# Kernel tuning notes

Hardware: AMD Instinct MI355X
Metric: run time of the kernel (lower is better)

Reference implementation:

```python
import jax, jax.numpy as jnp
import numpy as np

B, N, E, H, DEPTH = 2, 2048, 1024, 8, 12
D = E // H // 2  # head_dim = 64
LN_EPS = 1e-5


def setup_inputs() -> dict:
    key = jax.random.key(0)
    ks = jax.random.split(key, 10)
    w = lambda k: jax.random.normal(k, (E, E), jnp.float32) * (E ** -0.5)
    lp = lambda k: jax.random.normal(k, (D,), jnp.float32) * 0.1
    return {
        "x": jax.random.normal(ks[0], (B, N, E), jnp.float32),
        "Wq": w(ks[1]), "Wk": w(ks[2]), "Wv": w(ks[3]), "Wo": w(ks[4]),
        "lq1": lp(ks[5]), "lk1": lp(ks[6]), "lq2": lp(ks[7]), "lk2": lp(ks[8]),
        "ln_g": jnp.ones((2 * D,), jnp.float32),
        "ln_b": jnp.zeros((2 * D,), jnp.float32),
    }


def reference(x, Wq, Wk, Wv, Wo, lq1, lk1, lq2, lk2, ln_g, ln_b):
    b, n, e = x.shape
    lam_init = 0.8 - 0.6 * np.exp(-0.3 * DEPTH)  # lambda_init_fn(depth)
    # projections; split into 2H half-heads of dim D for q,k; H heads of dim 2D for v
    q = (x @ Wq).reshape(b, n, 2 * H, D).transpose(0, 2, 1, 3) * (D ** -0.5)  # [b,2H,n,D]
    k = (x @ Wk).reshape(b, n, 2 * H, D).transpose(0, 2, 1, 3)                # [b,2H,n,D]
    v = (x @ Wv).reshape(b, n, H, 2 * D).transpose(0, 2, 1, 3)                # [b,H,n,2D]
    scores = jnp.einsum('bhqd,bhkd->bhqk', q, k)                              # [b,2H,n,n]
    attn = jax.nn.softmax(scores, axis=-1).reshape(b, H, 2, n, n)
    lam = jnp.exp(jnp.sum(lq1 * lk1)) - jnp.exp(jnp.sum(lq2 * lk2)) + lam_init
    w_diff = attn[:, :, 0] - lam * attn[:, :, 1]                              # [b,H,n,n]
    o = jnp.einsum('bhqk,bhkd->bhqd', w_diff, v)                              # [b,H,n,2D]
    # per-head LayerNorm over channel dim 2D
    mu = o.mean(-1, keepdims=True)
    var = ((o - mu) ** 2).mean(-1, keepdims=True)
    o = (o - mu) * jax.lax.rsqrt(var + LN_EPS) * ln_g + ln_b
    o = o.transpose(0, 2, 1, 3).reshape(b, n, e)
    return o @ Wo
```

## Files before the change

### kernel.cpp

```cpp
#include <hip/hip_runtime.h>
#include <hip/hip_bf16.h>
#include <math.h>

#define B_ 2
#define N_ 2048
#define E_ 1024
#define H_ 8

typedef __attribute__((ext_vector_type(8))) short frag8;
typedef __attribute__((ext_vector_type(4))) float f32x4;
typedef __attribute__((ext_vector_type(16))) float f32x16;
typedef __attribute__((ext_vector_type(8))) unsigned short u16x8;

constexpr float LAM_INIT = 0.7836057665316245f;
constexpr float LOG2E = 1.4426950408889634f;
constexpr float EXP2_GUARD = -23.083120654f;

static __device__ __forceinline__ float fast_exp2(float x) {
#if __has_builtin(__builtin_amdgcn_exp2f)
  return __builtin_amdgcn_exp2f(x);
#else
  return exp2f(x);
#endif
}

static __device__ __forceinline__ ushort f2bf(float f) {
  union { float f; unsigned u; } v; v.f = f;
  unsigned r = (v.u + 0x7FFFu + ((v.u >> 16) & 1u)) >> 16;
  return (ushort)r;
}

static __device__ __forceinline__ unsigned pkbf(float a, float b) {
  __hip_bfloat162 h = __float22bfloat162_rn(make_float2(a, b));
  return *(unsigned*)&h;
}

static __device__ __forceinline__ void async16(const void* g, void* l) {
  __builtin_amdgcn_global_load_lds((const __attribute__((address_space(1))) void*)g,
                                   (__attribute__((address_space(3))) void*)l, 16, 0, 0);
}

static __device__ __forceinline__ frag8 mkfrag(unsigned p0, unsigned p1,
                                               unsigned p2, unsigned p3) {
  auto r02 = __builtin_amdgcn_permlane32_swap((int)p0, (int)p2, false, false);
  auto r13 = __builtin_amdgcn_permlane32_swap((int)p1, (int)p3, false, false);
  union { unsigned u[4]; frag8 f; } u;
  u.u[0] = (unsigned)r02[0];
  u.u[1] = (unsigned)r13[0];
  u.u[2] = (unsigned)r02[1];
  u.u[3] = (unsigned)r13[1];
  return u.f;
}

__global__ __launch_bounds__(256) void prep_kernel(
    const float* __restrict__ x,
    const float* __restrict__ Wq, const float* __restrict__ Wk,
    const float* __restrict__ Wv, const float* __restrict__ Wo,
    const float* __restrict__ lq1, const float* __restrict__ lk1,
    const float* __restrict__ lq2, const float* __restrict__ lk2,
    ushort* __restrict__ xb, ushort* __restrict__ wqkvt, ushort* __restrict__ wot,
    float* __restrict__ lam_out) {
  __shared__ ushort t[64][72];
  const int bx = blockIdx.x;
  const int tid = threadIdx.x;
  if (bx < 2048) {
    int i = bx * 256 + tid;
    const float4* sp = (const float4*)x + (size_t)i * 2;
    float4 a = sp[0], b = sp[1];
    u16x8 o;
    o[0] = f2bf(a.x); o[1] = f2bf(a.y); o[2] = f2bf(a.z); o[3] = f2bf(a.w);
    o[4] = f2bf(b.x); o[5] = f2bf(b.y); o[6] = f2bf(b.z); o[7] = f2bf(b.w);
    *(u16x8*)(xb + (size_t)i * 8) = o;
  } else if (bx < 3072) {
    int idx = bx - 2048;
    int sel = idx >> 8, rem = idx & 255;
    const float* W = (sel == 0) ? Wq : (sel == 1) ? Wk : (sel == 2) ? Wv : Wo;
    ushort* Wt = (sel < 3) ? (wqkvt + (size_t)sel * 1048576) : wot;
    const int c0 = (rem & 15) * 64, r0 = (rem >> 4) * 64;
    {
      int r = tid >> 2, cc = (tid & 3) * 16;
      const float* sp = W + (size_t)(r0 + r) * 1024 + c0 + cc;
      #pragma unroll
      for (int j = 0; j < 4; j++) {
        float4 a = *(const float4*)(sp + j * 4);
        t[cc + j * 4 + 0][r] = f2bf(a.x);
        t[cc + j * 4 + 1][r] = f2bf(a.y);
        t[cc + j * 4 + 2][r] = f2bf(a.z);
        t[cc + j * 4 + 3][r] = f2bf(a.w);
      }
    }
    __syncthreads();
    int c = tid >> 2, rr = (tid & 3) * 16;
    ushort* dp = Wt + (size_t)(c0 + c) * 1024 + r0 + rr;
    *(u16x8*)dp = *(u16x8*)&t[c][rr];
    *(u16x8*)(dp + 8) = *(u16x8*)&t[c][rr + 8];
  } else {
    if (tid < 64) {
      float t1 = lq1[tid] * lk1[tid];
      float t2 = lq2[tid] * lk2[tid];
      #pragma unroll
      for (int off = 32; off > 0; off >>= 1) {
        t1 += __shfl_down(t1, off);
        t2 += __shfl_down(t2, off);
      }
      if (tid == 0) lam_out[0] = expf(t1) - expf(t2) + LAM_INIT;
    }
  }
}

__global__ __launch_bounds__(256) void gemm_qkv(const ushort* __restrict__ xb,
                                                const ushort* __restrict__ wqkvt,
                                                ushort* __restrict__ qkb,
                                                ushort* __restrict__ vtb, float qscale) {
  __shared__ ushort As[4096];
  __shared__ ushort Bs[4096];
  const int id0 = blockIdx.x;
  const int id = (id0 & 7) * 96 + (id0 >> 3);
  const ushort* A; const ushort* Bt; ushort* C;
  int m0, n0, ldc;
  float sc;
  if (id < 512) {
    m0 = (id >> 4) * 128; n0 = (id & 15) * 128;
    A = xb; Bt = wqkvt; C = qkb; ldc = 2048;
    sc = (n0 < 1024) ? qscale : 1.0f;
  } else {
    int id2 = id - 512;
    m0 = (id2 & 7) * 128; n0 = (id2 >> 3) * 128;
    A = wqkvt + 2 * 1048576; Bt = xb; C = vtb; ldc = 4096;
    sc = 1.0f;
  }
  const int tid = threadIdx.x;
  const int w = tid >> 6, l = tid & 63;
  const int quad = l >> 4, col16 = l & 15;
  const int wm = (w & 1) * 64, wn = (w >> 1) * 64;
  const int lrow = l >> 2, lcol = (l & 3) * 8;

  f32x4 acc[4][4];
  #pragma unroll
  for (int mt = 0; mt < 4; mt++)
    #pragma unroll
    for (int nt = 0; nt < 4; nt++) acc[mt][nt] = (f32x4){0.f, 0.f, 0.f, 0.f};

  for (int k0 = 0; k0 < 1024; k0 += 32) {
    __syncthreads();
    #pragma unroll
    for (int i = 0; i < 4; i++) {
      int s = w * 4 + i;
      if (s < 8) {
        const ushort* gp = A + (size_t)(m0 + s * 16 + lrow) * 1024 + k0 + lcol;
        async16(gp, (char*)As + s * 1024);
      } else {
        int s2 = s - 8;
        const ushort* gp = Bt + (size_t)(n0 + s2 * 16 + lrow) * 1024 + k0 + lcol;
        async16(gp, (char*)Bs + s2 * 1024);
      }
    }
    __syncthreads();
    frag8 af[4], bfr[4];
    #pragma unroll
    for (int mt = 0; mt < 4; mt++)
      af[mt] = *(const frag8*)((const char*)As + (wm + mt * 16 + col16) * 64 + quad * 16);
    #pragma unroll
    for (int nt = 0; nt < 4; nt++)
      bfr[nt] = *(const frag8*)((const char*)Bs + (wn + nt * 16 + col16) * 64 + quad * 16);
    #pragma unroll
    for (int mt = 0; mt < 4; mt++)
      #pragma unroll
      for (int nt = 0; nt < 4; nt++)
        acc[mt][nt] = __builtin_amdgcn_mfma_f32_16x16x32_bf16(af[mt], bfr[nt], acc[mt][nt], 0, 0, 0);
  }

  #pragma unroll
  for (int mt = 0; mt < 4; mt++)
    #pragma unroll
    for (int r = 0; r < 4; r++) {
      int m = m0 + wm + mt * 16 + quad * 4 + r;
      #pragma unroll
      for (int nt = 0; nt < 4; nt++) {
        int n = n0 + wn + nt * 16 + col16;
        C[(size_t)m * ldc + n] = f2bf(acc[mt][nt][r] * sc);
      }
    }
}

__global__ __launch_bounds__(256) void gemm_out(const ushort* __restrict__ A,
                                                const ushort* __restrict__ Bt,
                                                float* __restrict__ Cp) {
  __shared__ ushort As[2048];
  __shared__ ushort Bs[4096];
  const int tid = threadIdx.x;
  const int w = tid >> 6, l = tid & 63;
  const int quad = l >> 4, col16 = l & 15;
  const int m0 = blockIdx.y * 64, n0 = blockIdx.x * 128;
  const int wm = (w & 1) * 32, wn = (w >> 1) * 64;
  const int lrow = l >> 2, lcol = (l & 3) * 8;

  f32x4 acc[2][4];
  #pragma unroll
  for (int mt = 0; mt < 2; mt++)
    #pragma unroll
    for (int nt = 0; nt < 4; nt++) acc[mt][nt] = (f32x4){0.f, 0.f, 0.f, 0.f};

  for (int k0 = 0; k0 < 1024; k0 += 32) {
    __syncthreads();
    #pragma unroll
    for (int i = 0; i < 3; i++) {
      int s = w * 3 + i;
      if (s < 4) {
        const ushort* gp = A + (size_t)(m0 + s * 16 + lrow) * 1024 + k0 + lcol;
        async16(gp, (char*)As + s * 1024);
      } else {
        int s2 = s - 4;
        const ushort* gp = Bt + (size_t)(n0 + s2 * 16 + lrow) * 1024 + k0 + lcol;
        async16(gp, (char*)Bs + s2 * 1024);
      }
    }
    __syncthreads();
    frag8 af[2], bfr[4];
    #pragma unroll
    for (int mt = 0; mt < 2; mt++)
      af[mt] = *(const frag8*)((const char*)As + (wm + mt * 16 + col16) * 64 + quad * 16);
    #pragma unroll
    for (int nt = 0; nt < 4; nt++)
      bfr[nt] = *(const frag8*)((const char*)Bs + (wn + nt * 16 + col16) * 64 + quad * 16);
    #pragma unroll
    for (int mt = 0; mt < 2; mt++)
      #pragma unroll
      for (int nt = 0; nt < 4; nt++)
        acc[mt][nt] = __builtin_amdgcn_mfma_f32_16x16x32_bf16(af[mt], bfr[nt], acc[mt][nt], 0, 0, 0);
  }

  #pragma unroll
  for (int mt = 0; mt < 2; mt++)
    #pragma unroll
    for (int r = 0; r < 4; r++) {
      int m = m0 + wm + mt * 16 + quad * 4 + r;
      #pragma unroll
      for (int nt = 0; nt < 4; nt++) {
        int n = n0 + wn + nt * 16 + col16;
        Cp[(size_t)m * 1024 + n] = acc[mt][nt][r];
      }
    }
}

__global__ __launch_bounds__(512, 2) void flash_kernel(const ushort* __restrict__ qk,
                                                       const ushort* __restrict__ vt,
                                                       const float* __restrict__ lam_p,
                                                       const float* __restrict__ ln_g,
                                                       const float* __restrict__ ln_b,
                                                       ushort* __restrict__ onorm) {
  const int L = blockIdx.x;
  const int hb = (L & 7) | (((L >> 3) & 1) << 3);
  const int qb = L >> 4;
  const int h = hb & 7, b = hb >> 3;

  const int tid = threadIdx.x;
  const int w = tid >> 6;
  const int hsel = w >> 2;
  const int h2 = 2 * h + hsel;
  const int lane31 = tid & 31, half = (tid & 63) >> 5;
  const int qloc = (w & 3) * 32 + lane31;
  const int i0 = qb * 128 + (w & 3) * 32;

  __shared__ char smem[131584];
  char* A0 = smem;
  char* A1 = smem + 32768;
  char* B0 = smem + 65536;
  char* B1 = smem + 98304;
  float* epi = (float*)smem;
  float* epi_l = (float*)(smem + 131072);

  const float lam = lam_p[0];

  frag8 qf[4];
  #pragma unroll
  for (int chk = 0; chk < 4; chk++) {
    const ushort* qp = qk + (size_t)(b * N_ + i0 + lane31) * 2048 +
                       h2 * 64 + chk * 16 + half * 8;
    qf[chk] = *(const frag8*)qp;
  }

  f32x16 o_[4];
  #pragma unroll
  for (int cm = 0; cm < 4; cm++)
    #pragma unroll
    for (int i = 0; i < 16; i++) o_[cm][i] = 0.f;
  float la0 = 0.f, la1 = 0.f;

  auto stage = [&](int k0, char* buf) {
    {
      int row = tid >> 3, sch = (tid & 7) ^ (row & 7);
      const ushort* kg = qk + (size_t)(b * N_ + k0 + row) * 2048 + 1024 + (2 * h) * 64 + sch * 8;
      async16(kg, buf + w * 1024);
    }
    {
      int row = tid >> 3, sch = (tid & 7) ^ (row & 7);
      const ushort* kg = qk + (size_t)(b * N_ + k0 + row) * 2048 + 1024 + (2 * h + 1) * 64 + sch * 8;
      async16(kg, buf + 8192 + w * 1024);
    }
    #pragma unroll
    for (int it = 0; it < 2; it++) {
      int j = it * 512 + tid;
      int row = j >> 3, sch = (j & 7) ^ (row & 7);
      const ushort* vg = vt + (size_t)(h * 128 + row) * 4096 + b * N_ + k0 + sch * 8;
      async16(vg, buf + 16384 + it * 8192 + w * 1024);
    }
  };

  auto compute = [&](const char* buf) {
    const char* Kb = buf + hsel * 8192;
    const char* Vb = buf + 16384;
    #pragma unroll
    for (int kh = 0; kh < 2; kh++) {
      f32x16 st;
      #pragma unroll
      for (int i = 0; i < 16; i++) st[i] = EXP2_GUARD;
      const int r = kh * 32 + lane31;
      __builtin_amdgcn_s_setprio(1);
      #pragma unroll
      for (int chk = 0; chk < 4; chk++) {
        frag8 a = *(const frag8*)(Kb + r * 128 + (((chk << 1) | half) ^ (r & 7)) * 16);
        st = __builtin_amdgcn_mfma_f32_32x32x16_bf16(a, qf[chk], st, 0, 0, 0);
      }
      __builtin_amdgcn_s_setprio(0);
      unsigned pk[8];
      #pragma unroll
      for (int p = 0; p < 8; p++) {
        float e0 = fast_exp2(st[2 * p]);
        float e1 = fast_exp2(st[2 * p + 1]);
        la0 += e0;
        la1 += e1;
        pk[p] = pkbf(e0, e1);
      }
      #pragma unroll
      for (int c16 = 0; c16 < 2; c16++) {
        frag8 bfr = mkfrag(pk[c16 * 4 + 0], pk[c16 * 4 + 1],
                           pk[c16 * 4 + 2], pk[c16 * 4 + 3]);
        __builtin_amdgcn_s_setprio(1);
        #pragma unroll
        for (int cm = 0; cm < 4; cm++) {
          int c = cm * 32 + lane31;
          int g = (kh * 4 + c16 * 2 + half) ^ (c & 7);
          frag8 a = *(const frag8*)(Vb + c * 128 + g * 16);
          o_[cm] = __builtin_amdgcn_mfma_f32_32x32x16_bf16(a, bfr, o_[cm], 0, 0, 0);
        }
        __builtin_amdgcn_s_setprio(0);
      }
    }
  };

  stage(0, A0);
  stage(64, A1);
  #pragma unroll 1
  for (int j = 0; j < 8; j++) {
    const int k0 = j * 256;
    __syncthreads();
    stage(k0 + 128, B0);
    stage(k0 + 192, B1);
    compute(A0);
    compute(A1);
    __syncthreads();
    if (j < 7) {
      stage(k0 + 256, A0);
      stage(k0 + 320, A1);
    }
    compute(B0);
    compute(B1);
  }

  float l_acc = la0 + la1;
  float lt = l_acc + __shfl_xor(l_acc, 32);

  if (hsel == 1) {
    if (half == 0) epi_l[qloc] = lt;
    #pragma unroll
    for (int cm = 0; cm < 4; cm++)
      #pragma unroll
      for (int g = 0; g < 4; g++) {
        int c = cm * 32 + g * 8 + half * 4;
        int pch = (c >> 2) ^ (qloc & 31);
        *(f32x4*)&epi[qloc * 128 + pch * 4] =
            (f32x4){o_[cm][4 * g + 0], o_[cm][4 * g + 1],
                    o_[cm][4 * g + 2], o_[cm][4 * g + 3]};
      }
  }
  __syncthreads();
  if (hsel == 0) {
    const float rle = 1.0f / lt;
    const float rlo = 1.0f / epi_l[qloc];
    float sum = 0.f, ss = 0.f;
    #pragma unroll
    for (int cm = 0; cm < 4; cm++)
      #pragma unroll
      for (int g = 0; g < 4; g++) {
        int c = cm * 32 + g * 8 + half * 4;
        int pch = (c >> 2) ^ (qloc & 31);
        f32x4 ov = *(const f32x4*)&epi[qloc * 128 + pch * 4];
        #pragma unroll
        for (int j = 0; j < 4; j++) {
          float v = o_[cm][4 * g + j] * rle - lam * ov[j] * rlo;
          o_[cm][4 * g + j] = v;
          sum += v;
          ss += v * v;
        }
      }
    sum += __shfl_xor(sum, 32);
    ss += __shfl_xor(ss, 32);
    float mu = sum * (1.0f / 128.0f);
    float var = ss * (1.0f / 128.0f) - mu * mu;
    float rr = rsqrtf(var + 1e-5f);
    int q = qb * 128 + qloc;
    ushort* ob = onorm + ((size_t)(b * N_ + q)) * E_ + h * 128;
    #pragma unroll
    for (int cm = 0; cm < 4; cm++)
      #pragma unroll
      for (int g = 0; g < 4; g++) {
        int c = cm * 32 + g * 8 + half * 4;
        float4 g4 = *(const float4*)&ln_g[c];
        float4 b4 = *(const float4*)&ln_b[c];
        float v0 = (o_[cm][4 * g + 0] - mu) * rr * g4.x + b4.x;
        float v1 = (o_[cm][4 * g + 1] - mu) * rr * g4.y + b4.y;
        float v2 = (o_[cm][4 * g + 2] - mu) * rr * g4.z + b4.z;
        float v3 = (o_[cm][4 * g + 3] - mu) * rr * g4.w + b4.w;
        uint2 pv;
        pv.x = pkbf(v0, v1);
        pv.y = pkbf(v2, v3);
        *(uint2*)(ob + c) = pv;
      }
  }
}

extern "C" void kernel_launch(void* const* d_in, const int* in_sizes, int n_in,
                              void* d_out, int out_size, void* d_ws, size_t ws_size,
                              hipStream_t stream) {
  const float* x    = (const float*)d_in[0];
  const float* Wq   = (const float*)d_in[1];
  const float* Wk   = (const float*)d_in[2];
  const float* Wv   = (const float*)d_in[3];
  const float* Wo   = (const float*)d_in[4];
  const float* lq1  = (const float*)d_in[5];
  const float* lk1  = (const float*)d_in[6];
  const float* lq2  = (const float*)d_in[7];
  const float* lk2  = (const float*)d_in[8];
  const float* ln_g = (const float*)d_in[9];
  const float* ln_b = (const float*)d_in[10];
  float* out = (float*)d_out;

  const size_t MN = (size_t)B_ * N_ * E_;
  ushort* xb    = (ushort*)d_ws;
  ushort* wqkvt = xb + MN;
  ushort* wot   = wqkvt + 3 * 1048576;
  ushort* qkb   = wot + 1048576;
  ushort* vtb   = qkb + (size_t)4096 * 2048;
  float*  lam   = (float*)(vtb + MN);
  ushort* onorm = xb;

  prep_kernel<<<dim3(3073), 256, 0, stream>>>(x, Wq, Wk, Wv, Wo, lq1, lk1, lq2, lk2,
                                              xb, wqkvt, wot, lam);

  gemm_qkv<<<dim3(768), 256, 0, stream>>>(xb, wqkvt, qkb, vtb, 0.125f * LOG2E);

  flash_kernel<<<dim3(256), 512, 0, stream>>>(qkb, vtb, lam, ln_g, ln_b, onorm);

  gemm_out<<<dim3(8, 64), 256, 0, stream>>>(onorm, wot, out);
}
```

Measured before the change: 211.7 us.

## Enlarge QKV GEMM tiles to 256x256 with double-buffered swizzled LDS

Rewrites the QKV projection GEMM to use 256x256 output tiles per 512-thread block, with a K step of 64 and two LDS buffers so the next tile's async loads overlap the current tile's MFMAs. LDS rows are XOR-swizzled to avoid bank conflicts, and s_setprio raises wave priority around the MFMA block. The larger tiles cut global reloads and sync count. The cost is 128KB of shared memory per block, heavy accumulator register use, and only 192 blocks, which is under one wave on 256 CUs.

```diff
diff --git a/kernel.cpp b/kernel.cpp
--- a/kernel.cpp
+++ b/kernel.cpp
@@ -108,77 +108,99 @@
   }
 }
 
-__global__ __launch_bounds__(256) void gemm_qkv(const ushort* __restrict__ xb,
-                                                const ushort* __restrict__ wqkvt,
-                                                ushort* __restrict__ qkb,
-                                                ushort* __restrict__ vtb, float qscale) {
-  __shared__ ushort As[4096];
-  __shared__ ushort Bs[4096];
+__global__ __launch_bounds__(512, 2) void gemm_qkv(const ushort* __restrict__ xb,
+                                                   const ushort* __restrict__ wqkvt,
+                                                   ushort* __restrict__ qkb,
+                                                   ushort* __restrict__ vtb, float qscale) {
+  __shared__ char smem[131072];
   const int id0 = blockIdx.x;
-  const int id = (id0 & 7) * 96 + (id0 >> 3);
-  const ushort* A; const ushort* Bt; ushort* C;
+  const int id = (id0 & 7) * 24 + (id0 >> 3);
+  const ushort* Ag; const ushort* Bg; ushort* C;
   int m0, n0, ldc;
   float sc;
-  if (id < 512) {
-    m0 = (id >> 4) * 128; n0 = (id & 15) * 128;
-    A = xb; Bt = wqkvt; C = qkb; ldc = 2048;
+  if (id < 128) {
+    m0 = (id >> 3) * 256; n0 = (id & 7) * 256;
+    Ag = xb; Bg = wqkvt; C = qkb; ldc = 2048;
     sc = (n0 < 1024) ? qscale : 1.0f;
   } else {
-    int id2 = id - 512;
-    m0 = (id2 & 7) * 128; n0 = (id2 >> 3) * 128;
-    A = wqkvt + 2 * 1048576; Bt = xb; C = vtb; ldc = 4096;
+    int id2 = id - 128;
+    m0 = (id2 & 3) * 256; n0 = (id2 >> 2) * 256;
+    Ag = wqkvt + 2 * 1048576; Bg = xb; C = vtb; ldc = 4096;
     sc = 1.0f;
   }
   const int tid = threadIdx.x;
   const int w = tid >> 6, l = tid & 63;
   const int quad = l >> 4, col16 = l & 15;
-  const int wm = (w & 1) * 64, wn = (w >> 1) * 64;
-  const int lrow = l >> 2, lcol = (l & 3) * 8;
-
-  f32x4 acc[4][4];
-  #pragma unroll
-  for (int mt = 0; mt < 4; mt++)
-    #pragma unroll
-    for (int nt = 0; nt < 4; nt++) acc[mt][nt] = (f32x4){0.f, 0.f, 0.f, 0.f};
-
-  for (int k0 = 0; k0 < 1024; k0 += 32) {
-    __syncthreads();
-    #pragma unroll
-    for (int i = 0; i < 4; i++) {
-      int s = w * 4 + i;
-      if (s < 8) {
-        const ushort* gp = A + (size_t)(m0 + s * 16 + lrow) * 1024 + k0 + lcol;
-        async16(gp, (char*)As + s * 1024);
-      } else {
-        int s2 = s - 8;
-        const ushort* gp = Bt + (size_t)(n0 + s2 * 16 + lrow) * 1024 + k0 + lcol;
-        async16(gp, (char*)Bs + s2 * 1024);
-      }
-    }
-    __syncthreads();
-    frag8 af[4], bfr[4];
-    #pragma unroll
-    for (int mt = 0; mt < 4; mt++)
-      af[mt] = *(const frag8*)((const char*)As + (wm + mt * 16 + col16) * 64 + quad * 16);
-    #pragma unroll
-    for (int nt = 0; nt < 4; nt++)
-      bfr[nt] = *(const frag8*)((const char*)Bs + (wn + nt * 16 + col16) * 64 + quad * 16);
-    #pragma unroll
-    for (int mt = 0; mt < 4; mt++)
-      #pragma unroll
-      for (int nt = 0; nt < 4; nt++)
-        acc[mt][nt] = __builtin_amdgcn_mfma_f32_16x16x32_bf16(af[mt], bfr[nt], acc[mt][nt], 0, 0, 0);
-  }
-
-  #pragma unroll
-  for (int mt = 0; mt < 4; mt++)
+  const int wr128 = (w >> 2) * 128;
+  const int wc64 = (w & 3) * 64;
+
+  f32x4 acc[8][4];
+  #pragma unroll
+  for (int mi = 0; mi < 8; mi++)
+    #pragma unroll
+    for (int nj = 0; nj < 4; nj++) acc[mi][nj] = (f32x4){0.f, 0.f, 0.f, 0.f};
+
+  auto stage = [&](int kt, char* buf) {
+    const int k0 = kt * 64;
+    #pragma unroll
+    for (int rr = 0; rr < 4; rr++) {
+      int e = rr * 512 + tid;
+      int row = e >> 3, slot = e & 7;
+      int ksw = k0 + ((slot ^ (row & 7)) << 3);
+      async16(Ag + (size_t)(m0 + row) * 1024 + ksw, buf + e * 16);
+      async16(Bg + (size_t)(n0 + row) * 1024 + ksw, buf + 32768 + e * 16);
+    }
+  };
+
+  auto compute = [&](const char* buf) {
+    const char* Ab = buf;
+    const char* Bb = buf + 32768;
+    frag8 bf_[4][2];
+    #pragma unroll
+    for (int nj = 0; nj < 4; nj++) {
+      int rb = wc64 + nj * 16 + col16;
+      #pragma unroll
+      for (int kk = 0; kk < 2; kk++) {
+        int slot = kk * 4 + quad;
+        bf_[nj][kk] = *(const frag8*)(Bb + rb * 128 + ((slot ^ (rb & 7)) << 4));
+      }
+    }
+    __builtin_amdgcn_s_setprio(1);
+    #pragma unroll
+    for (int mi = 0; mi < 8; mi++) {
+      int ra = wr128 + mi * 16 + col16;
+      frag8 a0 = *(const frag8*)(Ab + ra * 128 + ((quad ^ (ra & 7)) << 4));
+      frag8 a1 = *(const frag8*)(Ab + ra * 128 + (((4 + quad) ^ (ra & 7)) << 4));
+      #pragma unroll
+      for (int nj = 0; nj < 4; nj++) {
+        acc[mi][nj] = __builtin_amdgcn_mfma_f32_16x16x32_bf16(a0, bf_[nj][0], acc[mi][nj], 0, 0, 0);
+        acc[mi][nj] = __builtin_amdgcn_mfma_f32_16x16x32_bf16(a1, bf_[nj][1], acc[mi][nj], 0, 0, 0);
+      }
+    }
+    __builtin_amdgcn_s_setprio(0);
+  };
+
+  char* buf0 = smem;
+  char* buf1 = smem + 65536;
+  stage(0, buf0);
+  #pragma unroll 1
+  for (int kt = 0; kt < 16; kt++) {
+    char* cur = (kt & 1) ? buf1 : buf0;
+    char* nxt = (kt & 1) ? buf0 : buf1;
+    __syncthreads();
+    if (kt < 15) stage(kt + 1, nxt);
+    compute(cur);
+  }
+
+  #pragma unroll
+  for (int mi = 0; mi < 8; mi++)
     #pragma unroll
     for (int r = 0; r < 4; r++) {
-      int m = m0 + wm + mt * 16 + quad * 4 + r;
-      #pragma unroll
-      for (int nt = 0; nt < 4; nt++) {
-        int n = n0 + wn + nt * 16 + col16;
-        C[(size_t)m * ldc + n] = f2bf(acc[mt][nt][r] * sc);
+      int m = m0 + wr128 + mi * 16 + quad * 4 + r;
+      #pragma unroll
+      for (int nj = 0; nj < 4; nj++) {
+        int n = n0 + wc64 + nj * 16 + col16;
+        C[(size_t)m * ldc + n] = f2bf(acc[mi][nj][r] * sc);
       }
     }
 }
@@ -458,7 +480,7 @@
   prep_kernel<<<dim3(3073), 256, 0, stream>>>(x, Wq, Wk, Wv, Wo, lq1, lk1, lq2, lk2,
                                               xb, wqkvt, wot, lam);
 
-  gemm_qkv<<<dim3(768), 256, 0, stream>>>(xb, wqkvt, qkb, vtb, 0.125f * LOG2E);
+  gemm_qkv<<<dim3(192), 512, 0, stream>>>(xb, wqkvt, qkb, vtb, 0.125f * LOG2E);
 
   flash_kernel<<<dim3(256), 512, 0, stream>>>(qkb, vtb, lam, ln_g, ln_b, onorm);
 
```

New measurement: 207.7 us. No clear change (-1.9%).
